# Kernel optimization log

Hardware: AMD Instinct MI355X
Metric: run time of the kernel (lower is better)

Reference implementation:

```python
import jax, jax.numpy as jnp
import numpy as np

K = 5       # kernel_size
UP = 2      # up_factor
EPS = 1e-5  # BatchNorm eps (eval mode)


def _conv(x, w, pad, dil=1):
    return jax.lax.conv_general_dilated(
        x, w, (1, 1), [(pad, pad), (pad, pad)], rhs_dilation=(dil, dil),
        dimension_numbers=('NCHW', 'OIHW', 'NCHW'))


def _bn(x, g, b, m, v):
    inv = g / jnp.sqrt(v + EPS)
    return x * inv[:, None, None] + (b - m * inv)[:, None, None]


def _bilinear(x, oh, ow):
    # torch F.interpolate(mode='bilinear', align_corners=False)
    N, C, H, W = x.shape
    def coords(out_s, in_s):
        s = in_s / out_s
        src = (jnp.arange(out_s, dtype=jnp.float32) + 0.5) * s - 0.5
        src = jnp.clip(src, 0.0, in_s - 1)
        i0 = jnp.floor(src).astype(jnp.int32)
        i1 = jnp.minimum(i0 + 1, in_s - 1)
        return i0, i1, src - i0
    y0, y1, wy = coords(oh, H)
    x0, x1, wx = coords(ow, W)
    g = lambda yi, xi: x[:, :, yi][:, :, :, xi]  # (N,C,oh,ow)
    top = g(y0, x0) * (1 - wx) + g(y0, x1) * wx
    bot = g(y1, x0) * (1 - wx) + g(y1, x1) * wx
    return top * (1 - wy)[:, None] + bot * wy[:, None]


def _unfold(x):
    # F.unfold(k=5, pad=2) reshaped to (N, C, K*K, H, W); channel-major (c, kh, kw)
    p = K // 2
    N, C, H, W = x.shape
    xp = jnp.pad(x, ((0, 0), (0, 0), (p, p), (p, p)))
    patches = [xp[:, :, i:i + H, j:j + W] for i in range(K) for j in range(K)]
    return jnp.stack(patches, axis=2)


def setup_inputs() -> dict:
    key = jax.random.key(0)
    ks = jax.random.split(key, 8)
    N, C, H, W = 2, 256, 48, 48
    Cc = C // 4
    Cout = 256
    d = {}
    d['x'] = jax.random.normal(ks[0], (N, C, H, W), dtype=jnp.float32)
    d['compress_w'] = jax.random.normal(ks[1], (Cc, C, 1, 1), dtype=jnp.float32) * 0.05
    d['g1'] = jnp.ones((Cc,), jnp.float32)
    d['b1'] = jnp.zeros((Cc,), jnp.float32)
    d['m1'] = jax.random.normal(ks[2], (Cc,), dtype=jnp.float32) * 0.1
    d['v1'] = jax.random.uniform(ks[3], (Cc,), minval=0.5, maxval=1.5, dtype=jnp.float32)
    d['ke1_w'] = jax.random.normal(ks[4], (Cc, Cc, 3, 3), dtype=jnp.float32) * 0.05
    d['gk'] = jnp.ones((Cc,), jnp.float32)
    d['bk'] = jnp.zeros((Cc,), jnp.float32)
    d['mk'] = jax.random.normal(ks[5], (Cc,), dtype=jnp.float32) * 0.1
    d['vk'] = jax.random.uniform(ks[6], (Cc,), minval=0.5, maxval=1.5, dtype=jnp.float32)
    d['ke2_w'] = jax.random.normal(ks[7], (UP * UP * K * K, Cc, 3, 3), dtype=jnp.float32) * 0.05
    d['proj_w'] = jax.random.normal(jax.random.fold_in(key, 10), (Cout, C, 1, 1), dtype=jnp.float32) * 0.05
    d['g2'] = jnp.ones((Cout,), jnp.float32)
    d['b2'] = jnp.zeros((Cout,), jnp.float32)
    d['m2'] = jax.random.normal(jax.random.fold_in(key, 11), (Cout,), dtype=jnp.float32) * 0.1
    d['v2'] = jax.random.uniform(jax.random.fold_in(key, 12), (Cout,), minval=0.5, maxval=1.5, dtype=jnp.float32)
    return d


def reference(x, compress_w, g1, b1, m1, v1, ke1_w, gk, bk, mk, vk, ke2_w,
              proj_w, g2, b2, m2, v2):
    N, C, H, W = x.shape
    oh, ow = H * UP, W * UP
    # kernel prediction branch
    comp = jax.nn.relu(_bn(_conv(x, compress_w, 0), g1, b1, m1, v1))
    k1 = jax.nn.relu(_bn(_conv(comp, ke1_w, 2, dil=2), gk, bk, mk, vk))
    kernel = _conv(k1, ke2_w, 1)                               # (N, UP^2*K^2, H, W)
    kernel = jax.nn.softmax(kernel.reshape(N, UP * UP, K * K, H, W), axis=2)
    # content reassembly
    x_up = jnp.repeat(jnp.repeat(x, UP, axis=2), UP, axis=3)
    x_unf = _unfold(x_up)                                      # (N, C, K^2, oh, ow)
    k_up = _bilinear(kernel.reshape(N, UP * UP * K * K, H, W), oh, ow)
    k_up = k_up.reshape(N, UP * UP, K * K, oh, ow)
    out = jnp.einsum('nckhw,nukhw->nuchw', x_unf, k_up)        # (N, UP^2, C, oh, ow)
    # view (N, UP^2*C, oh, ow) then pixel_shuffle(UP)
    out = out.reshape(N, UP * UP * C, oh, ow)
    out = out.reshape(N, C, UP, UP, oh, ow)
    out = out.transpose(0, 1, 4, 2, 5, 3).reshape(N, C, oh * UP, ow * UP)
    out = jax.nn.relu(_bn(_conv(out, proj_w, 0), g2, b2, m2, v2))
    return out
```

## Files before the change

### kernel.cpp

```cpp
#include <hip/hip_runtime.h>

#define EPSB 1e-5f

typedef __attribute__((ext_vector_type(8))) short bf16x8;
typedef __attribute__((ext_vector_type(4))) float f32x4;

__device__ __forceinline__ unsigned short f2b(float f) {
  union { float f; unsigned u; } cv; cv.f = f;
  unsigned r = cv.u + 0x7FFFu + ((cv.u >> 16) & 1u);
  return (unsigned short)(r >> 16);
}

__global__ __launch_bounds__(256) void k_prep(
    const float* __restrict__ pw, const float* __restrict__ cw,
    const float* __restrict__ k1w, const float* __restrict__ k2w,
    const float* __restrict__ g1, const float* __restrict__ b1,
    const float* __restrict__ m1, const float* __restrict__ v1,
    const float* __restrict__ gk, const float* __restrict__ bk,
    const float* __restrict__ mk, const float* __restrict__ vk,
    const float* __restrict__ g2, const float* __restrict__ b2,
    const float* __restrict__ m2, const float* __restrict__ v2,
    unsigned short* __restrict__ pwb, unsigned short* __restrict__ wcb_t,
    unsigned short* __restrict__ wt1, unsigned short* __restrict__ wt2,
    float* __restrict__ sb1, float* __restrict__ sbk, float* __restrict__ sb2,
    float* __restrict__ wsz) {
  int i = blockIdx.x * 256 + threadIdx.x;
  if (i < 333056) wsz[i] = 0.f;
  if (i < 65536) pwb[i] = f2b(pw[i]);
  int j = i - 65536;
  if (j >= 0 && j < 16384) { int ci = j >> 6, co = j & 63; wcb_t[j] = f2b(cw[co * 256 + ci]); }
  int a = i - 81920;
  if (a >= 0 && a < 36864) {
    int co = a / 576, k = a % 576, tap = k >> 6, ci = k & 63;
    wt1[a] = f2b(k1w[co * 576 + ci * 9 + tap]);
  }
  int c2 = i - 118784;
  if (c2 >= 0 && c2 < 73728) {
    int co = c2 / 576, k = c2 % 576, tap = k >> 6, ci = k & 63;
    wt2[c2] = (co < 100) ? f2b(k2w[co * 576 + ci * 9 + tap]) : (unsigned short)0;
  }
  int s = i - 192512;
  if (s >= 0 && s < 64) { float iv = g1[s] / sqrtf(v1[s] + EPSB); sb1[s] = iv; sb1[64 + s] = b1[s] - m1[s] * iv; }
  if (s >= 64 && s < 128) { int c = s - 64; float iv = gk[c] / sqrtf(vk[c] + EPSB); sbk[c] = iv; sbk[64 + c] = bk[c] - mk[c] * iv; }
  if (s >= 128 && s < 384) { int c = s - 128; float iv = g2[c] / sqrtf(v2[c] + EPSB); sb2[c] = iv; sb2[256 + c] = b2[c] - m2[c] * iv; }
}

__global__ __launch_bounds__(256) void k_compress(
    const float* __restrict__ x, const unsigned short* __restrict__ wcb_t,
    const float* __restrict__ sb1, unsigned short* __restrict__ comp_t) {
  __shared__ unsigned short wl[16384];
  int t = threadIdx.x;
  for (int f = t; f < 2048; f += 256)
    *(bf16x8*)&wl[f * 8] = *(const bf16x8*)&wcb_t[f * 8];
  __syncthreads();
  int idx = blockIdx.x * 256 + t;
  int co2 = (idx & 31) * 2;
  int pg = idx >> 5;
  int n = pg / 1152;
  int pix0 = (pg % 1152) * 2;
  const float* xp = x + (size_t)n * 256 * 2304 + pix0;
  float a00 = 0.f, a01 = 0.f, a10 = 0.f, a11 = 0.f;
  for (int ci = 0; ci < 256; ++ci) {
    float2 xv = *(const float2*)(xp + (size_t)ci * 2304);
    unsigned pr = *(const unsigned*)&wl[ci * 64 + co2];
    union { unsigned u; float f; } wa, wb;
    wa.u = pr << 16; wb.u = pr & 0xffff0000u;
    a00 = fmaf(xv.x, wa.f, a00); a01 = fmaf(xv.y, wa.f, a01);
    a10 = fmaf(xv.x, wb.f, a10); a11 = fmaf(xv.y, wb.f, a11);
  }
  float s0 = sb1[co2], s1 = sb1[co2 + 1];
  float c0b = sb1[64 + co2], c1b = sb1[64 + co2 + 1];
  float o00 = fmaxf(fmaf(a00, s0, c0b), 0.f), o01 = fmaxf(fmaf(a01, s0, c0b), 0.f);
  float o10 = fmaxf(fmaf(a10, s1, c1b), 0.f), o11 = fmaxf(fmaf(a11, s1, c1b), 0.f);
  int r = pix0 / 48, c = pix0 % 48;
  unsigned short* ob = comp_t + ((size_t)n * 2704 + (r + 2) * 52 + (c + 2)) * 64 + co2;
  unsigned p0 = (unsigned)f2b(o00) | ((unsigned)f2b(o10) << 16);
  unsigned p1 = (unsigned)f2b(o01) | ((unsigned)f2b(o11) << 16);
  *(unsigned*)&ob[0]  = p0;
  *(unsigned*)&ob[64] = p1;
}

__global__ __launch_bounds__(256) void k_ke1(
    const unsigned short* __restrict__ comp_t, const unsigned short* __restrict__ wt1,
    const float* __restrict__ sbk, unsigned short* __restrict__ k1_t) {
  __shared__ unsigned short sA[16640];
  int t = threadIdx.x;
  int bid = blockIdx.x;
  int n = bid / 48, y = bid % 48;
  const unsigned short* src = comp_t + ((size_t)n * 52 + y) * 52 * 64;
  for (int f = t; f < 2080; f += 256) {
    int g = f >> 3, ci0 = (f & 7) * 8;
    int cc = g % 52, rr = g / 52;
    bf16x8 vv = *(const bf16x8*)&src[(rr * 52 + cc) * 64 + ci0];
    int ba = (((rr * 52 + cc) * 64 + ci0) * 2) ^ ((cc & 7) << 4);
    *(bf16x8*)((char*)sA + ba) = vv;
  }
  __syncthreads();
  int wid = t >> 6, l = t & 63, l15 = l & 15, lg = l >> 4;
  f32x4 acc[3];
  acc[0] = acc[1] = acc[2] = (f32x4){0.f, 0.f, 0.f, 0.f};
  const unsigned short* arow = wt1 + (size_t)(wid * 16 + l15) * 576;
#pragma unroll
  for (int kbi = 0; kbi < 18; ++kbi) {
    int tap = kbi >> 1;
    int ky = tap / 3, kx = tap % 3;
    int ci0 = (kbi & 1) * 32 + lg * 8;
    bf16x8 afr = *(const bf16x8*)&arow[kbi * 32 + lg * 8];
#pragma unroll
    for (int nt = 0; nt < 3; ++nt) {
      int col = nt * 16 + l15 + 2 * kx;
      int ba = (((2 * ky * 52 + col) * 64 + ci0) * 2) ^ ((col & 7) << 4);
      bf16x8 bfr = *(const bf16x8*)((char*)sA + ba);
      acc[nt] = __builtin_amdgcn_mfma_f32_16x16x32_bf16(afr, bfr, acc[nt], 0, 0, 0);
    }
  }
  unsigned short* dst = k1_t + ((size_t)n * 50 + (y + 1)) * 50 * 64;
  int co0 = wid * 16 + lg * 4;
  float s0 = sbk[co0], s1 = sbk[co0 + 1], s2 = sbk[co0 + 2], s3 = sbk[co0 + 3];
  float d0 = sbk[64 + co0], d1 = sbk[64 + co0 + 1], d2 = sbk[64 + co0 + 2], d3 = sbk[64 + co0 + 3];
#pragma unroll
  for (int nt = 0; nt < 3; ++nt) {
    int px = nt * 16 + l15;
    ushort4 pk;
    pk.x = f2b(fmaxf(fmaf(acc[nt][0], s0, d0), 0.f));
    pk.y = f2b(fmaxf(fmaf(acc[nt][1], s1, d1), 0.f));
    pk.z = f2b(fmaxf(fmaf(acc[nt][2], s2, d2), 0.f));
    pk.w = f2b(fmaxf(fmaf(acc[nt][3], s3, d3), 0.f));
    *(ushort4*)&dst[(px + 1) * 64 + co0] = pk;
  }
}

__global__ __launch_bounds__(256) void k_ke2(
    const unsigned short* __restrict__ k1_t, const unsigned short* __restrict__ wt2,
    float* __restrict__ kern_t) {
  __shared__ unsigned short sA[9600];
  int t = threadIdx.x;
  int bid = blockIdx.x;
  int n = bid / 48, y = bid % 48;
  const unsigned short* src = k1_t + ((size_t)n * 50 + y) * 50 * 64;
  for (int f = t; f < 1200; f += 256) {
    int g = f >> 3, ci0 = (f & 7) * 8;
    int cc = g % 50, rr = g / 50;
    bf16x8 vv = *(const bf16x8*)&src[(rr * 50 + cc) * 64 + ci0];
    int ba = (((rr * 50 + cc) * 64 + ci0) * 2) ^ ((cc & 7) << 4);
    *(bf16x8*)((char*)sA + ba) = vv;
  }
  __syncthreads();
  int wid = t >> 6, l = t & 63, l15 = l & 15, lg = l >> 4;
  f32x4 acc[2][3];
#pragma unroll
  for (int mi = 0; mi < 2; ++mi)
#pragma unroll
    for (int nt = 0; nt < 3; ++nt) acc[mi][nt] = (f32x4){0.f, 0.f, 0.f, 0.f};
#pragma unroll
  for (int kbi = 0; kbi < 18; ++kbi) {
    int tap = kbi >> 1;
    int ky = tap / 3, kx = tap % 3;
    int ci0 = (kbi & 1) * 32 + lg * 8;
    bf16x8 afr[2];
#pragma unroll
    for (int mi = 0; mi < 2; ++mi)
      afr[mi] = *(const bf16x8*)&wt2[(size_t)((wid * 2 + mi) * 16 + l15) * 576 + kbi * 32 + lg * 8];
#pragma unroll
    for (int nt = 0; nt < 3; ++nt) {
      int col = nt * 16 + l15 + kx;
      int ba = (((ky * 50 + col) * 64 + ci0) * 2) ^ ((col & 7) << 4);
      bf16x8 bfr = *(const bf16x8*)((char*)sA + ba);
      acc[0][nt] = __builtin_amdgcn_mfma_f32_16x16x32_bf16(afr[0], bfr, acc[0][nt], 0, 0, 0);
      acc[1][nt] = __builtin_amdgcn_mfma_f32_16x16x32_bf16(afr[1], bfr, acc[1][nt], 0, 0, 0);
    }
  }
#pragma unroll
  for (int mi = 0; mi < 2; ++mi) {
    int co0 = (wid * 2 + mi) * 16 + lg * 4;
    if (co0 < 100) {
#pragma unroll
      for (int nt = 0; nt < 3; ++nt) {
        int px = nt * 16 + l15;
        float4 vv = {acc[mi][nt][0], acc[mi][nt][1], acc[mi][nt][2], acc[mi][nt][3]};
        *(float4*)&kern_t[((size_t)n * 2304 + y * 48 + px) * 112 + co0] = vv;
      }
    }
  }
}

__global__ __launch_bounds__(256) void k_w9sm(const float* __restrict__ kern_t,
                                              float* __restrict__ w9) {
  __shared__ float ks[3 * 48 * 116];
  int bid = blockIdx.x;
  int n = bid / 48, k = bid % 48;
  int t = threadIdx.x;
  int rows[3] = {max(k - 1, 0), k, min(k + 1, 47)};
#pragma unroll
  for (int s = 0; s < 3; ++s) {
    const float* src = kern_t + ((size_t)n * 2304 + rows[s] * 48) * 112;
    for (int f = t; f < 1344; f += 256) {
      float4 vv = *(const float4*)&src[f * 4];
      int sx = f / 28, c = (f % 28) * 4;
      *(float4*)&ks[(s * 48 + sx) * 116 + c] = vv;
    }
  }
  __syncthreads();
#pragma unroll
  for (int it = 0; it < 3; ++it) {
    int f = t + it * 256;
    int half = f / 384, rem = f % 384;
    int w2 = rem >> 2, u = rem & 3;
    int y96 = 2 * k + half;
    float syf = fminf(fmaxf(y96 * 0.5f - 0.25f, 0.f), 47.f);
    int y0 = (int)syf; int y1 = min(y0 + 1, 47); float wy = syf - (float)y0;
    int sl0 = (y0 == k) ? 1 : 0;
    int sl1 = (y1 == k) ? 1 : 2;
    float sxf = fminf(fmaxf(w2 * 0.5f - 0.25f, 0.f), 47.f);
    int x0 = (int)sxf; int x1 = min(x0 + 1, 47); float wx = sxf - (float)x0;
    float bl[25];
#pragma unroll
    for (int kk = 0; kk < 25; ++kk) bl[kk] = 0.f;
    float ws4[4] = {(1.f - wx) * (1.f - wy), wx * (1.f - wy), (1.f - wx) * wy, wx * wy};
    int ssy[4] = {sl0, sl0, sl1, sl1};
    int ssx[4] = {x0, x1, x0, x1};
#pragma unroll
    for (int s = 0; s < 4; ++s) {
      const float* p = &ks[(ssy[s] * 48 + ssx[s]) * 116 + u * 25];
      float vv[25], mx = -3.4e38f;
#pragma unroll
      for (int kk = 0; kk < 25; ++kk) { vv[kk] = p[kk]; mx = fmaxf(mx, vv[kk]); }
      float sum = 0.f;
#pragma unroll
      for (int kk = 0; kk < 25; ++kk) { vv[kk] = __expf(vv[kk] - mx); sum += vv[kk]; }
      float rs = ws4[s] / sum;
#pragma unroll
      for (int kk = 0; kk < 25; ++kk) bl[kk] = fmaf(vv[kk], rs, bl[kk]);
    }
#pragma unroll
    for (int kh = 0; kh < 5; ++kh) {
      bool vy = (unsigned)(y96 + kh - 2) < 96u;
#pragma unroll
      for (int kw = 0; kw < 5; ++kw) {
        bool vx = (unsigned)(w2 + kw - 2) < 96u;
        if (!(vy && vx)) bl[kh * 5 + kw] = 0.f;
      }
    }
    int py = y96 & 1, px_ = w2 & 1;
    float cc0[5], cc1[5], cc2[5];
#pragma unroll
    for (int kh = 0; kh < 5; ++kh) {
      cc0[kh] = px_ ? bl[kh * 5 + 0] : bl[kh * 5 + 0] + bl[kh * 5 + 1];
      cc1[kh] = px_ ? bl[kh * 5 + 1] + bl[kh * 5 + 2] : bl[kh * 5 + 2] + bl[kh * 5 + 3];
      cc2[kh] = px_ ? bl[kh * 5 + 3] + bl[kh * 5 + 4] : bl[kh * 5 + 4];
    }
    float* op = w9 + (((size_t)(n * 96 + y96) * 96 + w2) * 4 + u) * 12;
    op[0] = py ? cc0[0] : cc0[0] + cc0[1];
    op[1] = py ? cc1[0] : cc1[0] + cc1[1];
    op[2] = py ? cc2[0] : cc2[0] + cc2[1];
    op[3] = py ? cc0[1] + cc0[2] : cc0[2] + cc0[3];
    op[4] = py ? cc1[1] + cc1[2] : cc1[2] + cc1[3];
    op[5] = py ? cc2[1] + cc2[2] : cc2[2] + cc2[3];
    op[6] = py ? cc0[3] + cc0[4] : cc0[4];
    op[7] = py ? cc1[3] + cc1[4] : cc1[4];
    op[8] = py ? cc2[3] + cc2[4] : cc2[4];
  }
}

__device__ __forceinline__ void compute_vals(
    const float* __restrict__ xls, const float* __restrict__ w9s,
    int c, int ch, int u, int jb, float* __restrict__ v0, float* __restrict__ v1) {
  int p = c & 1;
  const float* xc0 = &xls[((2 * p + 0) * 64 + ch) * 35];
  const float* xc1 = &xls[((2 * p + 1) * 64 + ch) * 35];
  int cbase = jb >> 1;
  float w60[3][6], w61[3][6];
#pragma unroll
  for (int ry = 0; ry < 3; ++ry)
#pragma unroll
    for (int cc = 0; cc < 6; ++cc) {
      w60[ry][cc] = xc0[ry * 11 + cbase + cc];
      w61[ry][cc] = xc1[ry * 11 + cbase + cc];
    }
  const float* wrow = &w9s[((c >> 1) * 16 + jb) * 48 + u * 12];
#pragma unroll
  for (int jj = 0; jj < 8; ++jj) {
    const float* wt = wrow + jj * 48;
    float4 wa = *(const float4*)wt;
    float4 wb = *(const float4*)(wt + 4);
    float w8 = wt[8];
    int cs = jj >> 1;
    float a0 = w60[0][cs] * wa.x;
    a0 = fmaf(w60[0][cs + 1], wa.y, a0);
    a0 = fmaf(w60[0][cs + 2], wa.z, a0);
    a0 = fmaf(w60[1][cs],     wa.w, a0);
    a0 = fmaf(w60[1][cs + 1], wb.x, a0);
    a0 = fmaf(w60[1][cs + 2], wb.y, a0);
    a0 = fmaf(w60[2][cs],     wb.z, a0);
    a0 = fmaf(w60[2][cs + 1], wb.w, a0);
    a0 = fmaf(w60[2][cs + 2], w8,   a0);
    float a1 = w61[0][cs] * wa.x;
    a1 = fmaf(w61[0][cs + 1], wa.y, a1);
    a1 = fmaf(w61[0][cs + 2], wa.z, a1);
    a1 = fmaf(w61[1][cs],     wa.w, a1);
    a1 = fmaf(w61[1][cs + 1], wb.x, a1);
    a1 = fmaf(w61[1][cs + 2], wb.y, a1);
    a1 = fmaf(w61[2][cs],     wb.z, a1);
    a1 = fmaf(w61[2][cs + 1], wb.w, a1);
    a1 = fmaf(w61[2][cs + 2], w8,   a1);
    v0[jj] = a0;
    v1[jj] = a1;
  }
}

__global__ __launch_bounds__(512, 4) void k_reassemble_proj(
    const float* __restrict__ x, const float* __restrict__ w9,
    const unsigned short* __restrict__ pwb, const float* __restrict__ sb2,
    float* __restrict__ out) {
  __shared__ float xls[256 * 35];
  __shared__ float w9s[1536];
  __shared__ float sb2s[512];
  __shared__ unsigned short finT[2][32 * 256];

  int blk = blockIdx.x;
  int n = blk / 288;
  int r = blk % 288;
  int y48 = r / 6;
  int xt = r % 6;
  int X0 = xt * 32;
  int x480 = xt * 8;
  int t = threadIdx.x;

  sb2s[t] = sb2[t];
  {
    const float* wbase = w9 + ((size_t)(n * 96 + 2 * y48) * 96 + xt * 16) * 48;
    for (int f = t; f < 1536; f += 512) {
      int half = f / 768, o = f - half * 768;
      w9s[f] = wbase[(size_t)half * 4608 + o];
    }
  }
  const float* xb = x + (size_t)n * 256 * 2304;
  for (int f = t; f < 8448; f += 512) {
    int c = f / 33, rc = f - c * 33;
    int ry = rc / 11, cx = rc - ry * 11;
    int sy = min(max(y48 + ry - 1, 0), 47);
    int sx = min(max(x480 + cx - 1, 0), 47);
    int slot = (c & 3) * 64 + (c >> 2);
    xls[slot * 35 + rc] = xb[(size_t)c * 2304 + sy * 48 + sx];
  }
  __syncthreads();

  int ci = t & 255, half = t >> 8;
  int u = ci >> 6, ch = ci & 63;
  int cb = ci >> 3, crr = ci & 7;
  int jb = half * 8;
  int wid = t >> 6, l = t & 63, l15 = l & 15, lg = l >> 4;
  const unsigned short* a0p = pwb + (size_t)(wid * 2 * 16 + l15) * 256;
  const unsigned short* a1p = a0p + 16 * 256;
  size_t outn = (size_t)n * 256 * 36864;
  int Ybase = 4 * y48;

  float v0[8], v1[8];
  compute_vals(xls, w9s, 0, ch, u, jb, v0, v1);
#pragma unroll
  for (int jj = 0; jj < 8; ++jj) {
    int px0 = 2 * (jb + jj), px1 = px0 + 1;
    finT[0][px0 * 256 + ((cb ^ (px0 & 7)) * 8 + crr)] = f2b(v0[jj]);
    finT[0][px1 * 256 + ((cb ^ (px1 & 7)) * 8 + crr)] = f2b(v1[jj]);
  }
  __syncthreads();

#pragma unroll
  for (int c = 0; c < 4; ++c) {
    f32x4 acc[2][2];
#pragma unroll
    for (int mi = 0; mi < 2; ++mi)
#pragma unroll
      for (int nt = 0; nt < 2; ++nt) acc[mi][nt] = (f32x4){0.f, 0.f, 0.f, 0.f};
#pragma unroll
    for (int kbi = 0; kbi < 8; ++kbi) {
      bf16x8 afr0 = *(const bf16x8*)&a0p[kbi * 32 + lg * 8];
      bf16x8 afr1 = *(const bf16x8*)&a1p[kbi * 32 + lg * 8];
      int cbk = kbi * 4 + lg;
#pragma unroll
      for (int nt = 0; nt < 2; ++nt) {
        int row = nt * 16 + l15;
        bf16x8 bfr = *(const bf16x8*)&finT[c & 1][row * 256 + ((cbk ^ (row & 7)) * 8)];
        acc[0][nt] = __builtin_amdgcn_mfma_f32_16x16x32_bf16(afr0, bfr, acc[0][nt], 0, 0, 0);
        acc[1][nt] = __builtin_amdgcn_mfma_f32_16x16x32_bf16(afr1, bfr, acc[1][nt], 0, 0, 0);
      }
    }
    if (c < 3) compute_vals(xls, w9s, c + 1, ch, u, jb, v0, v1);
    {
      float* orow = out + outn + (size_t)(Ybase + c) * 192 + X0;
#pragma unroll
      for (int mi = 0; mi < 2; ++mi) {
#pragma unroll
        for (int r4 = 0; r4 < 4; ++r4) {
          int o = (wid * 2 + mi) * 16 + lg * 4 + r4;
          float sc = sb2s[o], bi = sb2s[256 + o];
#pragma unroll
          for (int nt = 0; nt < 2; ++nt) {
            float val = fmaxf(fmaf(acc[mi][nt][r4], sc, bi), 0.f);
            orow[(size_t)o * 36864 + nt * 16 + l15] = val;
          }
        }
      }
    }
    if (c < 3) {
#pragma unroll
      for (int jj = 0; jj < 8; ++jj) {
        int px0 = 2 * (jb + jj), px1 = px0 + 1;
        finT[(c + 1) & 1][px0 * 256 + ((cb ^ (px0 & 7)) * 8 + crr)] = f2b(v0[jj]);
        finT[(c + 1) & 1][px1 * 256 + ((cb ^ (px1 & 7)) * 8 + crr)] = f2b(v1[jj]);
      }
      __syncthreads();
    }
  }
}

extern "C" void kernel_launch(void* const* d_in, const int* in_sizes, int n_in,
                              void* d_out, int out_size, void* d_ws, size_t ws_size,
                              hipStream_t stream) {
  const float* x   = (const float*)d_in[0];
  const float* cw  = (const float*)d_in[1];
  const float* g1  = (const float*)d_in[2];
  const float* b1  = (const float*)d_in[3];
  const float* m1  = (const float*)d_in[4];
  const float* v1  = (const float*)d_in[5];
  const float* k1w = (const float*)d_in[6];
  const float* gk  = (const float*)d_in[7];
  const float* bk  = (const float*)d_in[8];
  const float* mk  = (const float*)d_in[9];
  const float* vk  = (const float*)d_in[10];
  const float* k2w = (const float*)d_in[11];
  const float* pw  = (const float*)d_in[12];
  const float* g2  = (const float*)d_in[13];
  const float* b2  = (const float*)d_in[14];
  const float* m2  = (const float*)d_in[15];
  const float* v2  = (const float*)d_in[16];
  float* out = (float*)d_out;
  float* ws  = (float*)d_ws;

  unsigned short* comp_t = (unsigned short*)ws;
  unsigned short* k1_t   = (unsigned short*)(ws + 173056);
  float* kern_t = ws + 333056;
  float* w9     = ws + 849152;
  unsigned short* pwb   = (unsigned short*)(ws + 1733888);
  unsigned short* wcb_t = (unsigned short*)(ws + 1766656);
  unsigned short* wt1   = (unsigned short*)(ws + 1774848);
  unsigned short* wt2   = (unsigned short*)(ws + 1793280);
  float* sb1 = ws + 1830144;
  float* sbk = ws + 1830272;
  float* sb2 = ws + 1830400;

  k_prep<<<1302, 256, 0, stream>>>(pw, cw, k1w, k2w, g1, b1, m1, v1,
                                   gk, bk, mk, vk, g2, b2, m2, v2,
                                   pwb, wcb_t, wt1, wt2, sb1, sbk, sb2, ws);
  k_compress<<<288, 256, 0, stream>>>(x, wcb_t, sb1, comp_t);
  k_ke1<<<96, 256, 0, stream>>>(comp_t, wt1, sbk, k1_t);
  k_ke2<<<96, 256, 0, stream>>>(k1_t, wt2, kern_t);
  k_w9sm<<<96, 256, 0, stream>>>(kern_t, w9);
  k_reassemble_proj<<<576, 512, 0, stream>>>(x, w9, pwb, sb2, out);
}
```

Measured before the change: 230.5 us.

## Fuse prep into compress, fold softmax/bilinear into reassembly, split ke convs

Merges weight conversion and BN folding into the compress kernel and the conv kernels. It zeroes only the padding halos instead of the whole workspace. The softmax and bilinear kernel-weight computation (w9) moves into the final reassembly+projection kernel, which recomputes it from kern_t in shared memory. This removes two launches and the w9 global round trip. ke1/ke2 now split output channels across twice as many 128-thread blocks for more parallelism, and compute_write stores straight to LDS without staging registers. The cost is redundant BN and softmax recomputation per block and a larger shared-memory footprint.

```diff
diff --git a/kernel.cpp b/kernel.cpp
--- a/kernel.cpp
+++ b/kernel.cpp
@@ -11,84 +11,94 @@
   return (unsigned short)(r >> 16);
 }
 
-__global__ __launch_bounds__(256) void k_prep(
-    const float* __restrict__ pw, const float* __restrict__ cw,
-    const float* __restrict__ k1w, const float* __restrict__ k2w,
+__global__ __launch_bounds__(256) void k_head(
+    const float* __restrict__ x, const float* __restrict__ cw,
     const float* __restrict__ g1, const float* __restrict__ b1,
     const float* __restrict__ m1, const float* __restrict__ v1,
+    const float* __restrict__ k1w, const float* __restrict__ k2w,
+    const float* __restrict__ pw,
+    unsigned short* __restrict__ comp_t, unsigned short* __restrict__ pwb,
+    unsigned short* __restrict__ wt1, unsigned short* __restrict__ wt2) {
+  int bid = blockIdx.x, t = threadIdx.x;
+  if (bid < 288) {
+    __shared__ unsigned short wl[16640];
+    for (int f = t; f < 16384; f += 256) {
+      int co = f >> 8, ci = f & 255;
+      wl[ci * 65 + co] = f2b(cw[f]);
+    }
+    __syncthreads();
+    int idx = bid * 256 + t;
+    int co2 = (idx & 31) * 2;
+    int pg = idx >> 5;
+    int n = pg / 1152;
+    int pix0 = (pg % 1152) * 2;
+    const float* xp = x + (size_t)n * 256 * 2304 + pix0;
+    float a00 = 0.f, a01 = 0.f, a10 = 0.f, a11 = 0.f;
+    for (int ci = 0; ci < 256; ++ci) {
+      float2 xv = *(const float2*)(xp + (size_t)ci * 2304);
+      unsigned pr = *(const unsigned*)&wl[ci * 65 + co2];
+      union { unsigned u; float f; } wa, wb;
+      wa.u = pr << 16; wb.u = pr & 0xffff0000u;
+      a00 = fmaf(xv.x, wa.f, a00); a01 = fmaf(xv.y, wa.f, a01);
+      a10 = fmaf(xv.x, wb.f, a10); a11 = fmaf(xv.y, wb.f, a11);
+    }
+    float iv0 = g1[co2] / sqrtf(v1[co2] + EPSB);
+    float iv1 = g1[co2 + 1] / sqrtf(v1[co2 + 1] + EPSB);
+    float c0b = b1[co2] - m1[co2] * iv0;
+    float c1b = b1[co2 + 1] - m1[co2 + 1] * iv1;
+    float o00 = fmaxf(fmaf(a00, iv0, c0b), 0.f), o01 = fmaxf(fmaf(a01, iv0, c0b), 0.f);
+    float o10 = fmaxf(fmaf(a10, iv1, c1b), 0.f), o11 = fmaxf(fmaf(a11, iv1, c1b), 0.f);
+    int r = pix0 / 48, c = pix0 % 48;
+    unsigned short* ob = comp_t + ((size_t)n * 2704 + (r + 2) * 52 + (c + 2)) * 64 + co2;
+    *(unsigned*)&ob[0]  = (unsigned)f2b(o00) | ((unsigned)f2b(o10) << 16);
+    *(unsigned*)&ob[64] = (unsigned)f2b(o01) | ((unsigned)f2b(o11) << 16);
+  } else if (bid < 388) {
+    int i = (bid - 288) * 256 + t;
+    int n = i / 12800, r = i % 12800;
+    int bp = r >> 5, c32 = r & 31;
+    int rr, cc;
+    if (bp < 104) { rr = bp / 52; cc = bp % 52; }
+    else if (bp >= 296) { rr = 50 + (bp - 296) / 52; cc = (bp - 296) % 52; }
+    else { int q = bp - 104; rr = 2 + (q >> 2); int c4 = q & 3; cc = (c4 < 2) ? c4 : c4 + 48; }
+    ((unsigned*)comp_t)[((size_t)n * 2704 + rr * 52 + cc) * 32 + c32] = 0u;
+  } else {
+    int i2 = (bid - 388) * 256 + t;
+    if (i2 < 65536) {
+      pwb[i2] = f2b(pw[i2]);
+    } else if (i2 < 102400) {
+      int a = i2 - 65536;
+      int co = a / 576, k = a % 576, tap = k >> 6, ci = k & 63;
+      wt1[a] = f2b(k1w[co * 576 + ci * 9 + tap]);
+    } else {
+      int c2 = i2 - 102400;
+      int co = c2 / 576, k = c2 % 576, tap = k >> 6, ci = k & 63;
+      wt2[c2] = (co < 100) ? f2b(k2w[co * 576 + ci * 9 + tap]) : (unsigned short)0;
+    }
+  }
+}
+
+__global__ __launch_bounds__(128) void k_ke1(
+    const unsigned short* __restrict__ comp_t, const unsigned short* __restrict__ wt1,
     const float* __restrict__ gk, const float* __restrict__ bk,
     const float* __restrict__ mk, const float* __restrict__ vk,
-    const float* __restrict__ g2, const float* __restrict__ b2,
-    const float* __restrict__ m2, const float* __restrict__ v2,
-    unsigned short* __restrict__ pwb, unsigned short* __restrict__ wcb_t,
-    unsigned short* __restrict__ wt1, unsigned short* __restrict__ wt2,
-    float* __restrict__ sb1, float* __restrict__ sbk, float* __restrict__ sb2,
-    float* __restrict__ wsz) {
-  int i = blockIdx.x * 256 + threadIdx.x;
-  if (i < 333056) wsz[i] = 0.f;
-  if (i < 65536) pwb[i] = f2b(pw[i]);
-  int j = i - 65536;
-  if (j >= 0 && j < 16384) { int ci = j >> 6, co = j & 63; wcb_t[j] = f2b(cw[co * 256 + ci]); }
-  int a = i - 81920;
-  if (a >= 0 && a < 36864) {
-    int co = a / 576, k = a % 576, tap = k >> 6, ci = k & 63;
-    wt1[a] = f2b(k1w[co * 576 + ci * 9 + tap]);
-  }
-  int c2 = i - 118784;
-  if (c2 >= 0 && c2 < 73728) {
-    int co = c2 / 576, k = c2 % 576, tap = k >> 6, ci = k & 63;
-    wt2[c2] = (co < 100) ? f2b(k2w[co * 576 + ci * 9 + tap]) : (unsigned short)0;
-  }
-  int s = i - 192512;
-  if (s >= 0 && s < 64) { float iv = g1[s] / sqrtf(v1[s] + EPSB); sb1[s] = iv; sb1[64 + s] = b1[s] - m1[s] * iv; }
-  if (s >= 64 && s < 128) { int c = s - 64; float iv = gk[c] / sqrtf(vk[c] + EPSB); sbk[c] = iv; sbk[64 + c] = bk[c] - mk[c] * iv; }
-  if (s >= 128 && s < 384) { int c = s - 128; float iv = g2[c] / sqrtf(v2[c] + EPSB); sb2[c] = iv; sb2[256 + c] = b2[c] - m2[c] * iv; }
-}
-
-__global__ __launch_bounds__(256) void k_compress(
-    const float* __restrict__ x, const unsigned short* __restrict__ wcb_t,
-    const float* __restrict__ sb1, unsigned short* __restrict__ comp_t) {
-  __shared__ unsigned short wl[16384];
-  int t = threadIdx.x;
-  for (int f = t; f < 2048; f += 256)
-    *(bf16x8*)&wl[f * 8] = *(const bf16x8*)&wcb_t[f * 8];
-  __syncthreads();
-  int idx = blockIdx.x * 256 + t;
-  int co2 = (idx & 31) * 2;
-  int pg = idx >> 5;
-  int n = pg / 1152;
-  int pix0 = (pg % 1152) * 2;
-  const float* xp = x + (size_t)n * 256 * 2304 + pix0;
-  float a00 = 0.f, a01 = 0.f, a10 = 0.f, a11 = 0.f;
-  for (int ci = 0; ci < 256; ++ci) {
-    float2 xv = *(const float2*)(xp + (size_t)ci * 2304);
-    unsigned pr = *(const unsigned*)&wl[ci * 64 + co2];
-    union { unsigned u; float f; } wa, wb;
-    wa.u = pr << 16; wb.u = pr & 0xffff0000u;
-    a00 = fmaf(xv.x, wa.f, a00); a01 = fmaf(xv.y, wa.f, a01);
-    a10 = fmaf(xv.x, wb.f, a10); a11 = fmaf(xv.y, wb.f, a11);
-  }
-  float s0 = sb1[co2], s1 = sb1[co2 + 1];
-  float c0b = sb1[64 + co2], c1b = sb1[64 + co2 + 1];
-  float o00 = fmaxf(fmaf(a00, s0, c0b), 0.f), o01 = fmaxf(fmaf(a01, s0, c0b), 0.f);
-  float o10 = fmaxf(fmaf(a10, s1, c1b), 0.f), o11 = fmaxf(fmaf(a11, s1, c1b), 0.f);
-  int r = pix0 / 48, c = pix0 % 48;
-  unsigned short* ob = comp_t + ((size_t)n * 2704 + (r + 2) * 52 + (c + 2)) * 64 + co2;
-  unsigned p0 = (unsigned)f2b(o00) | ((unsigned)f2b(o10) << 16);
-  unsigned p1 = (unsigned)f2b(o01) | ((unsigned)f2b(o11) << 16);
-  *(unsigned*)&ob[0]  = p0;
-  *(unsigned*)&ob[64] = p1;
-}
-
-__global__ __launch_bounds__(256) void k_ke1(
-    const unsigned short* __restrict__ comp_t, const unsigned short* __restrict__ wt1,
-    const float* __restrict__ sbk, unsigned short* __restrict__ k1_t) {
+    unsigned short* __restrict__ k1_t) {
+  int bid = blockIdx.x, t = threadIdx.x;
+  if (bid >= 192) {
+    int j = (bid - 192) * 128 + t;
+    int n = j / 6272, r = j % 6272;
+    int bp = r >> 5, c32 = r & 31;
+    int rr, cc;
+    if (bp < 50) { rr = 0; cc = bp; }
+    else if (bp >= 146) { rr = 49; cc = bp - 146; }
+    else { int q = bp - 50; rr = 1 + (q >> 1); cc = (q & 1) * 49; }
+    ((unsigned*)k1_t)[((size_t)n * 2500 + rr * 50 + cc) * 32 + c32] = 0u;
+    return;
+  }
   __shared__ unsigned short sA[16640];
-  int t = threadIdx.x;
-  int bid = blockIdx.x;
-  int n = bid / 48, y = bid % 48;
+  int n = bid / 96, rem = bid % 96;
+  int y = rem >> 1, coh = rem & 1;
   const unsigned short* src = comp_t + ((size_t)n * 52 + y) * 52 * 64;
-  for (int f = t; f < 2080; f += 256) {
+  for (int f = t; f < 2080; f += 128) {
     int g = f >> 3, ci0 = (f & 7) * 8;
     int cc = g % 52, rr = g / 52;
     bf16x8 vv = *(const bf16x8*)&src[(rr * 52 + cc) * 64 + ci0];
@@ -99,7 +109,7 @@
   int wid = t >> 6, l = t & 63, l15 = l & 15, lg = l >> 4;
   f32x4 acc[3];
   acc[0] = acc[1] = acc[2] = (f32x4){0.f, 0.f, 0.f, 0.f};
-  const unsigned short* arow = wt1 + (size_t)(wid * 16 + l15) * 576;
+  const unsigned short* arow = wt1 + (size_t)(coh * 32 + wid * 16 + l15) * 576;
 #pragma unroll
   for (int kbi = 0; kbi < 18; ++kbi) {
     int tap = kbi >> 1;
@@ -115,9 +125,15 @@
     }
   }
   unsigned short* dst = k1_t + ((size_t)n * 50 + (y + 1)) * 50 * 64;
-  int co0 = wid * 16 + lg * 4;
-  float s0 = sbk[co0], s1 = sbk[co0 + 1], s2 = sbk[co0 + 2], s3 = sbk[co0 + 3];
-  float d0 = sbk[64 + co0], d1 = sbk[64 + co0 + 1], d2 = sbk[64 + co0 + 2], d3 = sbk[64 + co0 + 3];
+  int co0 = coh * 32 + wid * 16 + lg * 4;
+  float s0 = gk[co0] / sqrtf(vk[co0] + EPSB);
+  float s1 = gk[co0 + 1] / sqrtf(vk[co0 + 1] + EPSB);
+  float s2 = gk[co0 + 2] / sqrtf(vk[co0 + 2] + EPSB);
+  float s3 = gk[co0 + 3] / sqrtf(vk[co0 + 3] + EPSB);
+  float d0 = bk[co0] - mk[co0] * s0;
+  float d1 = bk[co0 + 1] - mk[co0 + 1] * s1;
+  float d2 = bk[co0 + 2] - mk[co0 + 2] * s2;
+  float d3 = bk[co0 + 3] - mk[co0 + 3] * s3;
 #pragma unroll
   for (int nt = 0; nt < 3; ++nt) {
     int px = nt * 16 + l15;
@@ -130,15 +146,15 @@
   }
 }
 
-__global__ __launch_bounds__(256) void k_ke2(
+__global__ __launch_bounds__(128) void k_ke2(
     const unsigned short* __restrict__ k1_t, const unsigned short* __restrict__ wt2,
     float* __restrict__ kern_t) {
   __shared__ unsigned short sA[9600];
-  int t = threadIdx.x;
-  int bid = blockIdx.x;
-  int n = bid / 48, y = bid % 48;
+  int bid = blockIdx.x, t = threadIdx.x;
+  int n = bid / 96, rem = bid % 96;
+  int y = rem >> 1, coh = rem & 1;
   const unsigned short* src = k1_t + ((size_t)n * 50 + y) * 50 * 64;
-  for (int f = t; f < 1200; f += 256) {
+  for (int f = t; f < 1200; f += 128) {
     int g = f >> 3, ci0 = (f & 7) * 8;
     int cc = g % 50, rr = g / 50;
     bf16x8 vv = *(const bf16x8*)&src[(rr * 50 + cc) * 64 + ci0];
@@ -160,7 +176,7 @@
     bf16x8 afr[2];
 #pragma unroll
     for (int mi = 0; mi < 2; ++mi)
-      afr[mi] = *(const bf16x8*)&wt2[(size_t)((wid * 2 + mi) * 16 + l15) * 576 + kbi * 32 + lg * 8];
+      afr[mi] = *(const bf16x8*)&wt2[(size_t)(coh * 64 + (wid * 2 + mi) * 16 + l15) * 576 + kbi * 32 + lg * 8];
 #pragma unroll
     for (int nt = 0; nt < 3; ++nt) {
       int col = nt * 16 + l15 + kx;
@@ -172,8 +188,8 @@
   }
 #pragma unroll
   for (int mi = 0; mi < 2; ++mi) {
-    int co0 = (wid * 2 + mi) * 16 + lg * 4;
-    if (co0 < 100) {
+    int co0 = coh * 64 + (wid * 2 + mi) * 16 + lg * 4;
+    if (co0 < 112) {
 #pragma unroll
       for (int nt = 0; nt < 3; ++nt) {
         int px = nt * 16 + l15;
@@ -184,87 +200,10 @@
   }
 }
 
-__global__ __launch_bounds__(256) void k_w9sm(const float* __restrict__ kern_t,
-                                              float* __restrict__ w9) {
-  __shared__ float ks[3 * 48 * 116];
-  int bid = blockIdx.x;
-  int n = bid / 48, k = bid % 48;
-  int t = threadIdx.x;
-  int rows[3] = {max(k - 1, 0), k, min(k + 1, 47)};
-#pragma unroll
-  for (int s = 0; s < 3; ++s) {
-    const float* src = kern_t + ((size_t)n * 2304 + rows[s] * 48) * 112;
-    for (int f = t; f < 1344; f += 256) {
-      float4 vv = *(const float4*)&src[f * 4];
-      int sx = f / 28, c = (f % 28) * 4;
-      *(float4*)&ks[(s * 48 + sx) * 116 + c] = vv;
-    }
-  }
-  __syncthreads();
-#pragma unroll
-  for (int it = 0; it < 3; ++it) {
-    int f = t + it * 256;
-    int half = f / 384, rem = f % 384;
-    int w2 = rem >> 2, u = rem & 3;
-    int y96 = 2 * k + half;
-    float syf = fminf(fmaxf(y96 * 0.5f - 0.25f, 0.f), 47.f);
-    int y0 = (int)syf; int y1 = min(y0 + 1, 47); float wy = syf - (float)y0;
-    int sl0 = (y0 == k) ? 1 : 0;
-    int sl1 = (y1 == k) ? 1 : 2;
-    float sxf = fminf(fmaxf(w2 * 0.5f - 0.25f, 0.f), 47.f);
-    int x0 = (int)sxf; int x1 = min(x0 + 1, 47); float wx = sxf - (float)x0;
-    float bl[25];
-#pragma unroll
-    for (int kk = 0; kk < 25; ++kk) bl[kk] = 0.f;
-    float ws4[4] = {(1.f - wx) * (1.f - wy), wx * (1.f - wy), (1.f - wx) * wy, wx * wy};
-    int ssy[4] = {sl0, sl0, sl1, sl1};
-    int ssx[4] = {x0, x1, x0, x1};
-#pragma unroll
-    for (int s = 0; s < 4; ++s) {
-      const float* p = &ks[(ssy[s] * 48 + ssx[s]) * 116 + u * 25];
-      float vv[25], mx = -3.4e38f;
-#pragma unroll
-      for (int kk = 0; kk < 25; ++kk) { vv[kk] = p[kk]; mx = fmaxf(mx, vv[kk]); }
-      float sum = 0.f;
-#pragma unroll
-      for (int kk = 0; kk < 25; ++kk) { vv[kk] = __expf(vv[kk] - mx); sum += vv[kk]; }
-      float rs = ws4[s] / sum;
-#pragma unroll
-      for (int kk = 0; kk < 25; ++kk) bl[kk] = fmaf(vv[kk], rs, bl[kk]);
-    }
-#pragma unroll
-    for (int kh = 0; kh < 5; ++kh) {
-      bool vy = (unsigned)(y96 + kh - 2) < 96u;
-#pragma unroll
-      for (int kw = 0; kw < 5; ++kw) {
-        bool vx = (unsigned)(w2 + kw - 2) < 96u;
-        if (!(vy && vx)) bl[kh * 5 + kw] = 0.f;
-      }
-    }
-    int py = y96 & 1, px_ = w2 & 1;
-    float cc0[5], cc1[5], cc2[5];
-#pragma unroll
-    for (int kh = 0; kh < 5; ++kh) {
-      cc0[kh] = px_ ? bl[kh * 5 + 0] : bl[kh * 5 + 0] + bl[kh * 5 + 1];
-      cc1[kh] = px_ ? bl[kh * 5 + 1] + bl[kh * 5 + 2] : bl[kh * 5 + 2] + bl[kh * 5 + 3];
-      cc2[kh] = px_ ? bl[kh * 5 + 3] + bl[kh * 5 + 4] : bl[kh * 5 + 4];
-    }
-    float* op = w9 + (((size_t)(n * 96 + y96) * 96 + w2) * 4 + u) * 12;
-    op[0] = py ? cc0[0] : cc0[0] + cc0[1];
-    op[1] = py ? cc1[0] : cc1[0] + cc1[1];
-    op[2] = py ? cc2[0] : cc2[0] + cc2[1];
-    op[3] = py ? cc0[1] + cc0[2] : cc0[2] + cc0[3];
-    op[4] = py ? cc1[1] + cc1[2] : cc1[2] + cc1[3];
-    op[5] = py ? cc2[1] + cc2[2] : cc2[2] + cc2[3];
-    op[6] = py ? cc0[3] + cc0[4] : cc0[4];
-    op[7] = py ? cc1[3] + cc1[4] : cc1[4];
-    op[8] = py ? cc2[3] + cc2[4] : cc2[4];
-  }
-}
-
-__device__ __forceinline__ void compute_vals(
+__device__ __forceinline__ void compute_write(
     const float* __restrict__ xls, const float* __restrict__ w9s,
-    int c, int ch, int u, int jb, float* __restrict__ v0, float* __restrict__ v1) {
+    unsigned short* __restrict__ ftbuf,
+    int c, int ch, int u, int jb, int cb, int crr) {
   int p = c & 1;
   const float* xc0 = &xls[((2 * p + 0) * 64 + ch) * 35];
   const float* xc1 = &xls[((2 * p + 1) * 64 + ch) * 35];
@@ -294,6 +233,8 @@
     a0 = fmaf(w60[2][cs],     wb.z, a0);
     a0 = fmaf(w60[2][cs + 1], wb.w, a0);
     a0 = fmaf(w60[2][cs + 2], w8,   a0);
+    int px0 = 2 * (jb + jj);
+    ftbuf[px0 * 256 + ((cb ^ (px0 & 7)) * 8 + crr)] = f2b(a0);
     float a1 = w61[0][cs] * wa.x;
     a1 = fmaf(w61[0][cs + 1], wa.y, a1);
     a1 = fmaf(w61[0][cs + 2], wa.z, a1);
@@ -303,36 +244,41 @@
     a1 = fmaf(w61[2][cs],     wb.z, a1);
     a1 = fmaf(w61[2][cs + 1], wb.w, a1);
     a1 = fmaf(w61[2][cs + 2], w8,   a1);
-    v0[jj] = a0;
-    v1[jj] = a1;
-  }
-}
-
-__global__ __launch_bounds__(512, 4) void k_reassemble_proj(
-    const float* __restrict__ x, const float* __restrict__ w9,
-    const unsigned short* __restrict__ pwb, const float* __restrict__ sb2,
+    int px1 = px0 + 1;
+    ftbuf[px1 * 256 + ((cb ^ (px1 & 7)) * 8 + crr)] = f2b(a1);
+  }
+}
+
+__global__ __launch_bounds__(512, 4) void k_fused(
+    const float* __restrict__ x, const float* __restrict__ kern_t,
+    const unsigned short* __restrict__ pwb,
+    const float* __restrict__ g2, const float* __restrict__ b2,
+    const float* __restrict__ m2, const float* __restrict__ v2,
     float* __restrict__ out) {
-  __shared__ float xls[256 * 35];
-  __shared__ float w9s[1536];
-  __shared__ float sb2s[512];
-  __shared__ unsigned short finT[2][32 * 256];
+  __shared__ __align__(16) char smem[76800];
+  float* xls  = (float*)smem;
+  float* w9s  = (float*)(smem + 35840);
+  float* sb2s = (float*)(smem + 41984);
+  unsigned short* finT0 = (unsigned short*)(smem + 44032);
+  float* ks   = (float*)(smem + 44032);
 
   int blk = blockIdx.x;
-  int n = blk / 288;
-  int r = blk % 288;
-  int y48 = r / 6;
-  int xt = r % 6;
-  int X0 = xt * 32;
-  int x480 = xt * 8;
+  int n = blk / 288, r = blk % 288;
+  int y48 = r / 6, xt = r % 6;
+  int X0 = xt * 32, x480 = xt * 8;
   int t = threadIdx.x;
 
-  sb2s[t] = sb2[t];
-  {
-    const float* wbase = w9 + ((size_t)(n * 96 + 2 * y48) * 96 + xt * 16) * 48;
-    for (int f = t; f < 1536; f += 512) {
-      int half = f / 768, o = f - half * 768;
-      w9s[f] = wbase[(size_t)half * 4608 + o];
-    }
+  if (t < 256) {
+    float iv = g2[t] / sqrtf(v2[t] + EPSB);
+    sb2s[t] = iv; sb2s[256 + t] = b2[t] - m2[t] * iv;
+  }
+  for (int f = t; f < 840; f += 512) {
+    int slot = f / 280, rem = f % 280;
+    int cx = rem / 28, c4 = rem % 28;
+    int sy = min(max(y48 + slot - 1, 0), 47);
+    int sx = min(max(x480 + cx - 1, 0), 47);
+    float4 vv = *(const float4*)&kern_t[((size_t)n * 2304 + sy * 48 + sx) * 112 + c4 * 4];
+    *(float4*)&ks[(slot * 10 + cx) * 112 + c4 * 4] = vv;
   }
   const float* xb = x + (size_t)n * 256 * 2304;
   for (int f = t; f < 8448; f += 512) {
@@ -345,24 +291,75 @@
   }
   __syncthreads();
 
+  {
+    int s = t & 3, tri = t >> 2;
+    int u = tri & 3, w2l = (tri >> 2) & 15, yhh = tri >> 6;
+    int y96 = 2 * y48 + yhh;
+    int w2 = xt * 16 + w2l;
+    float syf = fminf(fmaxf(y96 * 0.5f - 0.25f, 0.f), 47.f);
+    int y0 = (int)syf; float wy = syf - (float)y0; int y1 = min(y0 + 1, 47);
+    float sxf = fminf(fmaxf(w2 * 0.5f - 0.25f, 0.f), 47.f);
+    int x0 = (int)sxf; float wx = sxf - (float)x0; int x1 = min(x0 + 1, 47);
+    int slr = ((s & 2) ? y1 : y0) - y48 + 1;
+    int cxr = ((s & 1) ? x1 : x0) - x480 + 1;
+    float wgt = ((s & 1) ? wx : 1.f - wx) * ((s & 2) ? wy : 1.f - wy);
+    const float* p = &ks[(slr * 10 + cxr) * 112 + u * 25];
+    float bl[25], mx = -3.4e38f;
+#pragma unroll
+    for (int k = 0; k < 25; ++k) { bl[k] = p[k]; mx = fmaxf(mx, bl[k]); }
+    float sum = 0.f;
+#pragma unroll
+    for (int k = 0; k < 25; ++k) { bl[k] = __expf(bl[k] - mx); sum += bl[k]; }
+    float rs = wgt / sum;
+#pragma unroll
+    for (int k = 0; k < 25; ++k) {
+      bl[k] *= rs;
+      bl[k] += __shfl_xor(bl[k], 1);
+      bl[k] += __shfl_xor(bl[k], 2);
+    }
+    if (s == 0) {
+#pragma unroll
+      for (int kh = 0; kh < 5; ++kh) {
+        bool vy = (unsigned)(y96 + kh - 2) < 96u;
+#pragma unroll
+        for (int kw = 0; kw < 5; ++kw) {
+          bool vx = (unsigned)(w2 + kw - 2) < 96u;
+          if (!(vy && vx)) bl[kh * 5 + kw] = 0.f;
+        }
+      }
+      int py = yhh, px_ = w2l & 1;
+      float cc0[5], cc1[5], cc2[5];
+#pragma unroll
+      for (int kh = 0; kh < 5; ++kh) {
+        cc0[kh] = px_ ? bl[kh * 5 + 0] : bl[kh * 5 + 0] + bl[kh * 5 + 1];
+        cc1[kh] = px_ ? bl[kh * 5 + 1] + bl[kh * 5 + 2] : bl[kh * 5 + 2] + bl[kh * 5 + 3];
+        cc2[kh] = px_ ? bl[kh * 5 + 3] + bl[kh * 5 + 4] : bl[kh * 5 + 4];
+      }
+      float* op = &w9s[(yhh * 16 + w2l) * 48 + u * 12];
+      op[0] = py ? cc0[0] : cc0[0] + cc0[1];
+      op[1] = py ? cc1[0] : cc1[0] + cc1[1];
+      op[2] = py ? cc2[0] : cc2[0] + cc2[1];
+      op[3] = py ? cc0[1] + cc0[2] : cc0[2] + cc0[3];
+      op[4] = py ? cc1[1] + cc1[2] : cc1[2] + cc1[3];
+      op[5] = py ? cc2[1] + cc2[2] : cc2[2] + cc2[3];
+      op[6] = py ? cc0[3] + cc0[4] : cc0[4];
+      op[7] = py ? cc1[3] + cc1[4] : cc1[4];
+      op[8] = py ? cc2[3] + cc2[4] : cc2[4];
+    }
+  }
+  __syncthreads();
+
   int ci = t & 255, half = t >> 8;
   int u = ci >> 6, ch = ci & 63;
   int cb = ci >> 3, crr = ci & 7;
   int jb = half * 8;
   int wid = t >> 6, l = t & 63, l15 = l & 15, lg = l >> 4;
-  const unsigned short* a0p = pwb + (size_t)(wid * 2 * 16 + l15) * 256;
+  const unsigned short* a0p = pwb + (size_t)(wid * 32 + l15) * 256;
   const unsigned short* a1p = a0p + 16 * 256;
   size_t outn = (size_t)n * 256 * 36864;
   int Ybase = 4 * y48;
 
-  float v0[8], v1[8];
-  compute_vals(xls, w9s, 0, ch, u, jb, v0, v1);
-#pragma unroll
-  for (int jj = 0; jj < 8; ++jj) {
-    int px0 = 2 * (jb + jj), px1 = px0 + 1;
-    finT[0][px0 * 256 + ((cb ^ (px0 & 7)) * 8 + crr)] = f2b(v0[jj]);
-    finT[0][px1 * 256 + ((cb ^ (px1 & 7)) * 8 + crr)] = f2b(v1[jj]);
-  }
+  compute_write(xls, w9s, finT0, 0, ch, u, jb, cb, crr);
   __syncthreads();
 
 #pragma unroll
@@ -380,12 +377,12 @@
 #pragma unroll
       for (int nt = 0; nt < 2; ++nt) {
         int row = nt * 16 + l15;
-        bf16x8 bfr = *(const bf16x8*)&finT[c & 1][row * 256 + ((cbk ^ (row & 7)) * 8)];
+        bf16x8 bfr = *(const bf16x8*)&finT0[(c & 1) * 8192 + row * 256 + ((cbk ^ (row & 7)) * 8)];
         acc[0][nt] = __builtin_amdgcn_mfma_f32_16x16x32_bf16(afr0, bfr, acc[0][nt], 0, 0, 0);
         acc[1][nt] = __builtin_amdgcn_mfma_f32_16x16x32_bf16(afr1, bfr, acc[1][nt], 0, 0, 0);
       }
     }
-    if (c < 3) compute_vals(xls, w9s, c + 1, ch, u, jb, v0, v1);
+    if (c < 3) compute_write(xls, w9s, finT0 + ((c + 1) & 1) * 8192, c + 1, ch, u, jb, cb, crr);
     {
       float* orow = out + outn + (size_t)(Ybase + c) * 192 + X0;
 #pragma unroll
@@ -402,15 +399,7 @@
         }
       }
     }
-    if (c < 3) {
-#pragma unroll
-      for (int jj = 0; jj < 8; ++jj) {
-        int px0 = 2 * (jb + jj), px1 = px0 + 1;
-        finT[(c + 1) & 1][px0 * 256 + ((cb ^ (px0 & 7)) * 8 + crr)] = f2b(v0[jj]);
-        finT[(c + 1) & 1][px1 * 256 + ((cb ^ (px1 & 7)) * 8 + crr)] = f2b(v1[jj]);
-      }
-      __syncthreads();
-    }
+    if (c < 3) __syncthreads();
   }
 }
 
@@ -440,21 +429,13 @@
   unsigned short* comp_t = (unsigned short*)ws;
   unsigned short* k1_t   = (unsigned short*)(ws + 173056);
   float* kern_t = ws + 333056;
-  float* w9     = ws + 849152;
-  unsigned short* pwb   = (unsigned short*)(ws + 1733888);
-  unsigned short* wcb_t = (unsigned short*)(ws + 1766656);
-  unsigned short* wt1   = (unsigned short*)(ws + 1774848);
-  unsigned short* wt2   = (unsigned short*)(ws + 1793280);
-  float* sb1 = ws + 1830144;
-  float* sbk = ws + 1830272;
-  float* sb2 = ws + 1830400;
-
-  k_prep<<<1302, 256, 0, stream>>>(pw, cw, k1w, k2w, g1, b1, m1, v1,
-                                   gk, bk, mk, vk, g2, b2, m2, v2,
-                                   pwb, wcb_t, wt1, wt2, sb1, sbk, sb2, ws);
-  k_compress<<<288, 256, 0, stream>>>(x, wcb_t, sb1, comp_t);
-  k_ke1<<<96, 256, 0, stream>>>(comp_t, wt1, sbk, k1_t);
-  k_ke2<<<96, 256, 0, stream>>>(k1_t, wt2, kern_t);
-  k_w9sm<<<96, 256, 0, stream>>>(kern_t, w9);
-  k_reassemble_proj<<<576, 512, 0, stream>>>(x, w9, pwb, sb2, out);
-}
+  unsigned short* pwb = (unsigned short*)(ws + 849152);
+  unsigned short* wt1 = (unsigned short*)(ws + 881920);
+  unsigned short* wt2 = (unsigned short*)(ws + 900352);
+
+  k_head<<<1076, 256, 0, stream>>>(x, cw, g1, b1, m1, v1, k1w, k2w, pw,
+                                   comp_t, pwb, wt1, wt2);
+  k_ke1<<<290, 128, 0, stream>>>(comp_t, wt1, gk, bk, mk, vk, k1_t);
+  k_ke2<<<192, 128, 0, stream>>>(k1_t, wt2, kern_t);
+  k_fused<<<576, 512, 0, stream>>>(x, kern_t, pwb, g2, b2, m2, v2, out);
+}
```

New measurement: 231.3 us. About the same (+0.3%).
